# Kernel optimization log

Hardware: AMD Instinct MI355X
Metric: run time of the kernel (lower is better)

The kernel has to match this reference:

```python
import jax, jax.numpy as jnp
import numpy as np

IN_SHAPE, OUT_SHAPE = 512, 2048  # folding3 config from BSANet


def _sample_2d(m, n):
    # Faithful port of BSANet.sample_2D: 46x46 grid over [-0.3, 0.3]^2
    xs = np.linspace(-0.3, 0.3, 46)
    pts = np.stack(np.meshgrid(xs, xs))                    # [2, 46, 46]
    ix = np.round(np.linspace(0, 45, m)).astype(int)
    iy = np.round(np.linspace(0, 45, n)).astype(int)
    gx, gy = np.meshgrid(ix, iy)                           # each [n, m]
    return jnp.asarray(pts[:, gx.ravel(), gy.ravel()].T, jnp.float32)  # [m*n, 2]


def _lin(x, W, b):
    # MLP() in the source is Linear followed by ReLU for EVERY layer
    return jax.nn.relu(x @ W + b)


def setup_inputs() -> dict:
    key = jax.random.key(0)
    ks = jax.random.split(key, 20)
    def w(k, i, o):
        return jax.random.normal(k, (i, o), jnp.float32) / np.float32(np.sqrt(i))
    def bvec(k, o):
        return jax.random.normal(k, (o,), jnp.float32) * 0.01
    return {
        "p": jax.random.normal(ks[0], (32, IN_SHAPE, 128), jnp.float32),
        # SelfAttention MLPs (shared by both Up_module calls, as in the source)
        "Wh": w(ks[1], 256, 64),   "bh": bvec(ks[2], 64),
        "Wl": w(ks[3], 256, 64),   "bl": bvec(ks[4], 64),
        "Wg": w(ks[5], 256, 256),  "bg": bvec(ks[6], 256),
        "Wf": w(ks[7], 256, 128),  "bf": bvec(ks[8], 128),
        # M_up: MLP([130, 128])
        "Wup": w(ks[9], 130, 128), "bup": bvec(ks[10], 128),
        # M_down: MLP([512, 256, 128])
        "Wd1": w(ks[11], 512, 256), "bd1": bvec(ks[12], 256),
        "Wd2": w(ks[13], 256, 128), "bd2": bvec(ks[14], 128),
        "m": 64,
        "n": 32,
    }


def reference(p, Wh, bh, Wl, bl, Wg, bg, Wf, bf, Wup, bup, Wd1, bd1, Wd2, bd2, m, n):
    r = OUT_SHAPE // IN_SHAPE                              # 4
    pts = _sample_2d(m, n)                                 # [2048, 2]

    def up(q):                                             # q: [B, 512, 128]
        q = jnp.tile(q, (1, r, 1))                         # [B, 2048, 128] (torch repeat along dim 1)
        grid = jnp.broadcast_to(pts, (q.shape[0],) + pts.shape)
        q2d = _lin(jnp.concatenate([q, grid], -1), Wup, bup)   # [B, 2048, 128]
        qc = jnp.concatenate([q, q2d], -1)                 # [B, 2048, 256]
        h = _lin(qc, Wh, bh)                               # [B, 2048, 64]
        l = _lin(qc, Wl, bl)                               # [B, 2048, 64]
        g = _lin(qc, Wg, bg)                               # [B, 2048, 256]
        attn = jax.nn.softmax(jnp.einsum('bnd,bmd->bnm', l, h), axis=-1)  # [B, 2048, 2048]
        return _lin(qc + jnp.einsum('bnm,bmd->bnd', attn, g), Wf, bf)     # [B, 2048, 128]

    def down(q):                                           # q: [B, 2048, 128]
        q = q.reshape(q.shape[0], IN_SHAPE, r * q.shape[2])  # [B, 512, 512]
        return _lin(_lin(q, Wd1, bd1), Wd2, bd2)           # [B, 512, 128]

    p1 = up(p)
    p2 = up(p - down(p1))
    return p1 + p2
```

## Files before the change

### kernel.cpp

```cpp
#include <hip/hip_runtime.h>
#include <hip/hip_bf16.h>
#include <cmath>

#define NB   32
#define SOUT 2048
#define SIN  512
#define LOG2E 1.4426950408889634f

typedef __attribute__((ext_vector_type(8))) short bhalf8;
typedef __attribute__((ext_vector_type(4))) float f32x4;

__device__ inline ushort f2b(float x) {
  union { float f; unsigned u; } v; v.f = x;
  unsigned r = v.u + 0x7FFFu + ((v.u >> 16) & 1u);
  return (ushort)(r >> 16);
}
__device__ inline float b2f(ushort u) {
  union { unsigned u; float f; } v; v.u = ((unsigned)u) << 16;
  return v.f;
}
__device__ inline unsigned pkt(float lo, float hi) {
  union { float f; unsigned u; } a, b; a.f = lo; b.f = hi;
  return (a.u >> 16) | (b.u & 0xFFFF0000u);
}

__device__ inline void gload16(const void* g, void* l) {
  __builtin_amdgcn_global_load_lds(
      (const __attribute__((address_space(1))) void*)g,
      (__attribute__((address_space(3))) void*)l, 16, 0, 0);
}

__global__ void pts_kernel(const int* __restrict__ mArr, const int* __restrict__ nArr,
                           float* __restrict__ pts) {
  int k = blockIdx.x * blockDim.x + threadIdx.x;
  if (k >= SOUT) return;
  int m = mArr[0], n = nArr[0];
  int b = k % m, a = k / m;
  int ixb = (int)rint(45.0 * (double)b / (double)(m - 1));
  int iya = (int)rint(45.0 * (double)a / (double)(n - 1));
  const float step = 0.6f / 45.0f;
  pts[2 * k + 0] = -0.3f + step * (float)iya;
  pts[2 * k + 1] = -0.3f + step * (float)ixb;
}

__global__ __launch_bounds__(256) void wconv_kernel(
    const float* __restrict__ Wh, const float* __restrict__ Wl,
    const float* __restrict__ Wg, const float* __restrict__ Wf,
    const float* __restrict__ Wd1, const float* __restrict__ Wd2,
    const float* __restrict__ bh, const float* __restrict__ bl,
    const float* __restrict__ bg, const float* __restrict__ Wup,
    const float* __restrict__ bup, const float* __restrict__ pts,
    ushort* __restrict__ dst, float* __restrict__ fbias,
    float* __restrict__ gridterm) {
  const int which = blockIdx.y;
  int idx = blockIdx.x * 256 + threadIdx.x;
  if (which == 6) {
    if (idx < 384)
      fbias[idx] = idx < 64 ? bh[idx] : (idx < 128 ? bl[idx - 64] : bg[idx - 128]);
    return;
  }
  if (which == 7) {
    if (idx < 2048 * 128) {
      int i = idx >> 7, n = idx & 127;
      gridterm[idx] = bup[n] + pts[2 * i] * Wup[128 * 128 + n]
                             + pts[2 * i + 1] * Wup[129 * 128 + n];
    }
    return;
  }
  if (which == 8) {
    if (idx < 16384) {
      int n = idx >> 7, k = idx & 127;
      dst[294912 + n * 128 + k] = f2b(Wup[k * 128 + n]);
    }
    return;
  }
  const float* src; int K, N; long off;
  switch (which) {
    case 0: src = Wh;  K = 256; N = 64;  off = 0;      break;
    case 1: src = Wl;  K = 256; N = 64;  off = 16384;  break;
    case 2: src = Wg;  K = 256; N = 256; off = 32768;  break;
    case 3: src = Wf;  K = 256; N = 128; off = 98304;  break;
    case 4: src = Wd1; K = 512; N = 256; off = 131072; break;
    default:src = Wd2; K = 256; N = 128; off = 262144; break;
  }
  if (idx >= K * N) return;
  int n = idx / K, k = idx - n * K;
  dst[off + idx] = f2b(src[(long)k * N + n]);
}

__global__ __launch_bounds__(256) void pconv_kernel(
    const float* __restrict__ p, ushort* __restrict__ pb,
    ushort* __restrict__ qcb) {
  int idx = blockIdx.x * 256 + threadIdx.x;
  long base = (long)idx * 4;
  int b = (int)(base >> 16);
  int rem = (int)(base & 65535);
  int i = rem >> 7, n = rem & 127;
  float4 v = *(const float4*)(p + base);
  ushort4 u;
  u.x = f2b(v.x); u.y = f2b(v.y); u.z = f2b(v.z); u.w = f2b(v.w);
  *(ushort4*)(pb + base) = u;
#pragma unroll
  for (int j = 0; j < 4; ++j)
    *(ushort4*)(qcb + ((long)b * 2048 + i + 512 * j) * 256 + n) = u;
}

template <int MODE>
__global__ __launch_bounds__(256) void mgemm(
    const ushort* __restrict__ A, const ushort* __restrict__ Wt,
    const float* __restrict__ bias, void* __restrict__ outv,
    void* __restrict__ out2v, const float* __restrict__ aux,
    int M, int N, int K) {
  __shared__ alignas(16) ushort As[128 * 64];
  __shared__ alignas(16) ushort Bs[64 * 64];
  const int tid = threadIdx.x;
  const int w = tid >> 6, lane = tid & 63, g = lane >> 4, c = lane & 15;
  const int wm = w >> 1, wn = w & 1;
  const long row0 = (long)blockIdx.y * 128;
  const int col0 = blockIdx.x * 64;
  const long Astride = (long)K * 2;
  const char* Wb = (const char*)Wt;
  const long abase = (MODE == 6) ? ((row0 >> 11) * 512 + (row0 & 511)) : row0;
  const char* Ab = (const char*)A + abase * Astride;

  f32x4 acc[4][2];
#pragma unroll
  for (int i = 0; i < 4; ++i)
#pragma unroll
    for (int j = 0; j < 2; ++j) acc[i][j] = (f32x4){0.f, 0.f, 0.f, 0.f};

  for (int k0 = 0; k0 < K; k0 += 64) {
#pragma unroll
    for (int it = 0; it < 4; ++it) {
      int o = it * 4096 + w * 1024 + lane * 16;
      int row = o >> 7, cb = o & 127;
      gload16(Ab + (long)row * Astride + k0 * 2 + (cb ^ ((row & 7) << 4)),
              (char*)As + it * 4096 + w * 1024);
    }
#pragma unroll
    for (int it = 0; it < 2; ++it) {
      int o = it * 4096 + w * 1024 + lane * 16;
      int row = o >> 7, cb = o & 127;
      gload16(Wb + (long)(col0 + row) * Astride + k0 * 2 + (cb ^ ((row & 7) << 4)),
              (char*)Bs + it * 4096 + w * 1024);
    }
    __syncthreads();
#pragma unroll
    for (int koff = 0; koff < 2; ++koff) {
      bhalf8 a[4], bfr[2];
#pragma unroll
      for (int mi = 0; mi < 4; ++mi) {
        int row = 64 * wm + 16 * mi + c;
        a[mi] = *(const bhalf8*)((const char*)As + row * 128 +
                                 ((16 * g + 64 * koff) ^ ((row & 7) << 4)));
      }
#pragma unroll
      for (int ni = 0; ni < 2; ++ni) {
        int row = 32 * wn + 16 * ni + c;
        bfr[ni] = *(const bhalf8*)((const char*)Bs + row * 128 +
                                   ((16 * g + 64 * koff) ^ ((row & 7) << 4)));
      }
#pragma unroll
      for (int mi = 0; mi < 4; ++mi)
#pragma unroll
        for (int ni = 0; ni < 2; ++ni)
          acc[mi][ni] = __builtin_amdgcn_mfma_f32_16x16x32_bf16(a[mi], bfr[ni], acc[mi][ni], 0, 0, 0);
    }
    __syncthreads();
  }

#pragma unroll
  for (int ni = 0; ni < 2; ++ni) {
    int n = col0 + 32 * wn + 16 * ni + c;
    float bn = (MODE == 6) ? 0.f : bias[n];
#pragma unroll
    for (int mi = 0; mi < 4; ++mi) {
      long m0 = row0 + 64 * wm + 16 * mi + 4 * g;
      if (MODE == 6) {
        ushort* O = (ushort*)outv;
#pragma unroll
        for (int r = 0; r < 4; ++r) {
          int i2048 = (int)((m0 + r) & 2047);
          float val = fmaxf(acc[mi][ni][r] + aux[i2048 * 128 + n], 0.f);
          O[(m0 + r) * 256 + 128 + n] = f2b(val);
        }
        continue;
      }
      float v[4];
#pragma unroll
      for (int r = 0; r < 4; ++r) v[r] = fmaxf(acc[mi][ni][r] + bn, 0.f);
      if (MODE == 0) {
        ushort* O = (ushort*)outv;
#pragma unroll
        for (int r = 0; r < 4; ++r) O[(m0 + r) * N + n] = f2b(v[r]);
      } else if (MODE == 7) {
        if (n < 128) {
          ushort* O = (ushort*)outv;
          float sc = (n >= 64) ? LOG2E : 1.0f;
#pragma unroll
          for (int r = 0; r < 4; ++r) O[(m0 + r) * 128 + n] = f2b(v[r] * sc);
        } else {
          int bb = (int)(m0 >> 11);
          int ml = (int)(m0 & 2047);
          int d = n - 128;
          ushort4 u4;
          u4.x = f2b(v[0]); u4.y = f2b(v[1]); u4.z = f2b(v[2]); u4.w = f2b(v[3]);
          *(ushort4*)((ushort*)out2v + ((long)bb * 256 + d) * 2048 + ml) = u4;
        }
      } else if (MODE == 2) {
        ushort* O = (ushort*)outv;
        float* O2 = (float*)out2v;
#pragma unroll
        for (int r = 0; r < 4; ++r) {
          O2[(m0 + r) * N + n] = v[r];
          O[(m0 + r) * N + n] = f2b(v[r]);
        }
      } else if (MODE == 3) {
        ushort* Opmb = (ushort*)outv;
        ushort* Oqcb = (ushort*)out2v;
#pragma unroll
        for (int r = 0; r < 4; ++r) {
          float val = aux[(m0 + r) * N + n] - v[r];
          ushort uv = f2b(val);
          Opmb[(m0 + r) * 128 + n] = uv;
          long bb = (m0 + r) >> 9;
          int ii = (int)((m0 + r) & 511);
#pragma unroll
          for (int j = 0; j < 4; ++j)
            Oqcb[(bb * 2048 + ii + 512 * j) * 256 + n] = uv;
        }
      } else {
        float* O = (float*)outv;
#pragma unroll
        for (int r = 0; r < 4; ++r) O[(m0 + r) * N + n] = v[r] + aux[(m0 + r) * N + n];
      }
    }
  }
}

__global__ __launch_bounds__(256, 2) void attn_kernel(
    const ushort* __restrict__ hl, const ushort* __restrict__ gtm,
    ushort* __restrict__ qcb) {
  __shared__ alignas(16) ushort Ht[2][64 * 64];
  __shared__ alignas(16) ushort Gs[2][256 * 64];

  const int tid = threadIdx.x;
  const int w = tid >> 6, lane = tid & 63, g = lane >> 4, c = lane & 15;
  const int bid = blockIdx.x;
  const int wg = (bid & 7) * 64 + (bid >> 3);
  const int b = wg >> 4, nb = wg & 15;
  const float THR = 11.0f;

  bhalf8 la[2][2];
#pragma unroll
  for (int qg = 0; qg < 2; ++qg) {
    const ushort* lrow = hl + ((long)b * SOUT + nb * 128 + 32 * w + 16 * qg + c) * 128 + 64 + 8 * g;
    la[qg][0] = *(const bhalf8*)(lrow);
    la[qg][1] = *(const bhalf8*)(lrow + 32);
  }

  float mold[2] = {-INFINITY, -INFINITY}, srow[2] = {0.f, 0.f};
  f32x4 oacc[16][2];
#pragma unroll
  for (int t = 0; t < 16; ++t)
#pragma unroll
    for (int qg = 0; qg < 2; ++qg) oacc[t][qg] = (f32x4){0.f, 0.f, 0.f, 0.f};

  const char* hlbase = (const char*)(hl + (long)b * SOUT * 128);
  const char* gtb = (const char*)(gtm + (long)b * 256 * 2048);

  {
#pragma unroll
    for (int it = 0; it < 2; ++it) {
      int o = it * 4096 + tid * 16;
      int row = o >> 7, cb = o & 127;
      gload16(hlbase + row * 256 + (cb ^ ((row & 7) << 4)), (char*)Ht[0] + o);
    }
#pragma unroll
    for (int it = 0; it < 8; ++it) {
      int o = it * 4096 + tid * 16;
      int row = o >> 7, cb = o & 127;
      gload16(gtb + (long)row * 4096 + (cb ^ ((row & 7) << 4)), (char*)Gs[0] + o);
    }
  }
  __syncthreads();

  const int srcA = c + 32 * (g & 1);
  const int srcB = srcA + 16;
  const bool hi = (g >> 1) != 0;

  for (int mb = 0; mb < 32; ++mb) {
    const int buf = mb & 1;

    if (mb < 31) {
#pragma unroll
      for (int it = 0; it < 2; ++it) {
        int o = it * 4096 + tid * 16;
        int row = o >> 7, cb = o & 127;
        gload16(hlbase + ((long)(mb + 1) * 64 + row) * 256 + (cb ^ ((row & 7) << 4)),
                (char*)Ht[buf ^ 1] + o);
      }
#pragma unroll
      for (int it = 0; it < 8; ++it) {
        int o = it * 4096 + tid * 16;
        int row = o >> 7, cb = o & 127;
        gload16(gtb + (long)row * 4096 + (mb + 1) * 128 + (cb ^ ((row & 7) << 4)),
                (char*)Gs[buf ^ 1] + o);
      }
    }

    const char* hcur = (const char*)Ht[buf];
    f32x4 sacc[2][4];
#pragma unroll
    for (int qg = 0; qg < 2; ++qg)
#pragma unroll
      for (int j = 0; j < 4; ++j) sacc[qg][j] = (f32x4){0.f, 0.f, 0.f, 0.f};
#pragma unroll
    for (int j = 0; j < 4; ++j) {
      int row = 16 * j + c;
#pragma unroll
      for (int s = 0; s < 2; ++s) {
        bhalf8 hbf = *(const bhalf8*)(hcur + row * 128 +
                                      ((64 * s + 16 * g) ^ ((c & 7) << 4)));
        sacc[0][j] = __builtin_amdgcn_mfma_f32_16x16x32_bf16(hbf, la[0][s], sacc[0][j], 0, 0, 0);
        sacc[1][j] = __builtin_amdgcn_mfma_f32_16x16x32_bf16(hbf, la[1][s], sacc[1][j], 0, 0, 0);
      }
    }

    bhalf8 pb[2][2];
#pragma unroll
    for (int qg = 0; qg < 2; ++qg) {
      float mloc = sacc[qg][0][0];
#pragma unroll
      for (int j = 0; j < 4; ++j)
#pragma unroll
        for (int r = 0; r < 4; ++r) mloc = fmaxf(mloc, sacc[qg][j][r]);
      mloc = fmaxf(mloc, __shfl_xor(mloc, 16));
      mloc = fmaxf(mloc, __shfl_xor(mloc, 32));
      float mnew = fmaxf(mold[qg], mloc);
      bool keep = (mloc <= mold[qg] + THR);
      float scl = keep ? 1.0f : exp2f(mold[qg] - mnew);
      mold[qg] = keep ? mold[qg] : mnew;

      float psum = 0.f;
#pragma unroll
      for (int j = 0; j < 4; ++j)
#pragma unroll
        for (int r = 0; r < 4; ++r) {
          float e = exp2f(sacc[qg][j][r] - mold[qg]);
          sacc[qg][j][r] = e; psum += e;
        }
      psum += __shfl_xor(psum, 16);
      psum += __shfl_xor(psum, 32);
      srow[qg] = srow[qg] * scl + psum;
      if (!__all(keep)) {
#pragma unroll
        for (int t = 0; t < 16; ++t) {
          oacc[t][qg][0] *= scl; oacc[t][qg][1] *= scl;
          oacc[t][qg][2] *= scl; oacc[t][qg][3] *= scl;
        }
      }

#pragma unroll
      for (int s2 = 0; s2 < 2; ++s2) {
        int j2 = 2 * s2;
        unsigned wA0 = pkt(sacc[qg][j2][0], sacc[qg][j2][1]);
        unsigned wA1 = pkt(sacc[qg][j2][2], sacc[qg][j2][3]);
        unsigned wB0 = pkt(sacc[qg][j2 + 1][0], sacc[qg][j2 + 1][1]);
        unsigned wB1 = pkt(sacc[qg][j2 + 1][2], sacc[qg][j2 + 1][3]);
        unsigned a0A = (unsigned)__shfl((int)wA0, srcA);
        unsigned b0A = (unsigned)__shfl((int)wB0, srcA);
        unsigned a1A = (unsigned)__shfl((int)wA1, srcA);
        unsigned b1A = (unsigned)__shfl((int)wB1, srcA);
        unsigned a0B = (unsigned)__shfl((int)wA0, srcB);
        unsigned b0B = (unsigned)__shfl((int)wB0, srcB);
        unsigned a1B = (unsigned)__shfl((int)wA1, srcB);
        unsigned b1B = (unsigned)__shfl((int)wB1, srcB);
        union { unsigned u[4]; bhalf8 v; } pw;
        pw.u[0] = hi ? b0A : a0A;
        pw.u[1] = hi ? b1A : a1A;
        pw.u[2] = hi ? b0B : a0B;
        pw.u[3] = hi ? b1B : a1B;
        pb[qg][s2] = pw.v;
      }
    }

    const char* gcur = (const char*)Gs[buf];
#pragma unroll
    for (int s2 = 0; s2 < 2; ++s2) {
#pragma unroll
      for (int t = 0; t < 16; ++t) {
        int row = 16 * t + c;
        bhalf8 ga = *(const bhalf8*)(gcur + row * 128 +
                                     ((64 * s2 + 16 * g) ^ ((c & 7) << 4)));
        oacc[t][0] = __builtin_amdgcn_mfma_f32_16x16x32_bf16(ga, pb[0][s2], oacc[t][0], 0, 0, 0);
        oacc[t][1] = __builtin_amdgcn_mfma_f32_16x16x32_bf16(ga, pb[1][s2], oacc[t][1], 0, 0, 0);
      }
    }

    __syncthreads();
  }

#pragma unroll
  for (int qg = 0; qg < 2; ++qg) {
    float inv = 1.0f / srow[qg];
    long qrow = ((long)b * SOUT + nb * 128 + 32 * w + 16 * qg + c) * 256;
#pragma unroll
    for (int t = 0; t < 16; ++t) {
      long addr = qrow + 16 * t + 4 * g;
      ushort4 cur = *(const ushort4*)(qcb + addr);
      cur.x = f2b(b2f(cur.x) + oacc[t][qg][0] * inv);
      cur.y = f2b(b2f(cur.y) + oacc[t][qg][1] * inv);
      cur.z = f2b(b2f(cur.z) + oacc[t][qg][2] * inv);
      cur.w = f2b(b2f(cur.w) + oacc[t][qg][3] * inv);
      *(ushort4*)(qcb + addr) = cur;
    }
  }
}

extern "C" void kernel_launch(void* const* d_in, const int* in_sizes, int n_in,
                              void* d_out, int out_size, void* d_ws, size_t ws_size,
                              hipStream_t stream) {
  (void)in_sizes; (void)n_in; (void)out_size; (void)ws_size;
  const float* p   = (const float*)d_in[0];
  const float* Wh  = (const float*)d_in[1];
  const float* bh  = (const float*)d_in[2];
  const float* Wl  = (const float*)d_in[3];
  const float* bl  = (const float*)d_in[4];
  const float* Wg  = (const float*)d_in[5];
  const float* bg  = (const float*)d_in[6];
  const float* Wf  = (const float*)d_in[7];
  const float* bf  = (const float*)d_in[8];
  const float* Wup = (const float*)d_in[9];
  const float* bup = (const float*)d_in[10];
  const float* Wd1 = (const float*)d_in[11];
  const float* bd1 = (const float*)d_in[12];
  const float* Wd2 = (const float*)d_in[13];
  const float* bd2 = (const float*)d_in[14];
  const int* mArr  = (const int*)d_in[15];
  const int* nArr  = (const int*)d_in[16];
  float* out = (float*)d_out;

  float* ws       = (float*)d_ws;
  float* pts      = ws;
  float* p1       = ws + 4096;
  float* bhlg     = p1 + 8388608;
  float* gridterm = bhlg + 512;
  ushort* qcb  = (ushort*)(gridterm + 262144);
  ushort* hlb  = qcb + 16777216;
  ushort* gt   = hlb + 8388608;
  ushort* p1b  = gt + 16777216;
  ushort* d1b  = p1b + 8388608;
  ushort* pb   = d1b + 4194304;
  ushort* pmb  = pb + 2097152;
  ushort* wts  = pmb + 2097152;
  ushort* Wft  = wts + 98304;
  ushort* Wd1t = wts + 131072;
  ushort* Wd2t = wts + 262144;
  ushort* Wupt = wts + 294912;

  pts_kernel<<<8, 256, 0, stream>>>(mArr, nArr, pts);
  wconv_kernel<<<dim3(1024, 9), 256, 0, stream>>>(
      Wh, Wl, Wg, Wf, Wd1, Wd2, bh, bl, bg, Wup, bup, pts, wts, bhlg, gridterm);

  pconv_kernel<<<2048, 256, 0, stream>>>(p, pb, qcb);
  mgemm<6><<<dim3(2, 512), 256, 0, stream>>>(pb, Wupt, bhlg, qcb, nullptr, gridterm, 65536, 128, 128);
  mgemm<7><<<dim3(6, 512), 256, 0, stream>>>(qcb, wts, bhlg, hlb, gt, nullptr, 65536, 384, 256);
  attn_kernel<<<512, 256, 0, stream>>>(hlb, gt, qcb);
  mgemm<2><<<dim3(2, 512), 256, 0, stream>>>(qcb, Wft, bf, p1b, p1, nullptr, 65536, 128, 256);

  mgemm<0><<<dim3(4, 128), 256, 0, stream>>>(p1b, Wd1t, bd1, d1b, nullptr, nullptr, 16384, 256, 512);
  mgemm<3><<<dim3(2, 128), 256, 0, stream>>>(d1b, Wd2t, bd2, pmb, qcb, p, 16384, 128, 256);

  mgemm<6><<<dim3(2, 512), 256, 0, stream>>>(pmb, Wupt, bhlg, qcb, nullptr, gridterm, 65536, 128, 128);
  mgemm<7><<<dim3(6, 512), 256, 0, stream>>>(qcb, wts, bhlg, hlb, gt, nullptr, 65536, 384, 256);
  attn_kernel<<<512, 256, 0, stream>>>(hlb, gt, qcb);
  mgemm<4><<<dim3(2, 512), 256, 0, stream>>>(qcb, Wft, bf, out, p1, p1, 65536, 128, 256);
}
```

Baseline: 419.8 us.

## Single-buffer G tile in attention for higher occupancy; drop fp32 p1 copy

The attention kernel no longer double-buffers the 256x64 G tile in shared memory. It now loads G synchronously each iteration behind an extra barrier, which cuts LDS use and raises the launch-bounds occupancy target from 2 to 3 blocks per CU. The fp32 copy of p1 is also removed: the final GEMM adds the bf16 p1 instead, saving one fp32 write and read at some cost in precision. In exchange, the G load latency is no longer overlapped with the score computation and must be hidden by the extra occupancy.

```diff
diff --git a/kernel.cpp b/kernel.cpp
--- a/kernel.cpp
+++ b/kernel.cpp
@@ -207,14 +207,6 @@
           u4.x = f2b(v[0]); u4.y = f2b(v[1]); u4.z = f2b(v[2]); u4.w = f2b(v[3]);
           *(ushort4*)((ushort*)out2v + ((long)bb * 256 + d) * 2048 + ml) = u4;
         }
-      } else if (MODE == 2) {
-        ushort* O = (ushort*)outv;
-        float* O2 = (float*)out2v;
-#pragma unroll
-        for (int r = 0; r < 4; ++r) {
-          O2[(m0 + r) * N + n] = v[r];
-          O[(m0 + r) * N + n] = f2b(v[r]);
-        }
       } else if (MODE == 3) {
         ushort* Opmb = (ushort*)outv;
         ushort* Oqcb = (ushort*)out2v;
@@ -231,18 +223,20 @@
         }
       } else {
         float* O = (float*)outv;
-#pragma unroll
-        for (int r = 0; r < 4; ++r) O[(m0 + r) * N + n] = v[r] + aux[(m0 + r) * N + n];
-      }
-    }
-  }
-}
-
-__global__ __launch_bounds__(256, 2) void attn_kernel(
+        const ushort* auxb = (const ushort*)aux;
+#pragma unroll
+        for (int r = 0; r < 4; ++r)
+          O[(m0 + r) * N + n] = v[r] + b2f(auxb[(m0 + r) * N + n]);
+      }
+    }
+  }
+}
+
+__global__ __launch_bounds__(256, 3) void attn_kernel(
     const ushort* __restrict__ hl, const ushort* __restrict__ gtm,
     ushort* __restrict__ qcb) {
   __shared__ alignas(16) ushort Ht[2][64 * 64];
-  __shared__ alignas(16) ushort Gs[2][256 * 64];
+  __shared__ alignas(16) ushort Gs[256 * 64];
 
   const int tid = threadIdx.x;
   const int w = tid >> 6, lane = tid & 63, g = lane >> 4, c = lane & 15;
@@ -269,29 +263,28 @@
   const char* hlbase = (const char*)(hl + (long)b * SOUT * 128);
   const char* gtb = (const char*)(gtm + (long)b * 256 * 2048);
 
-  {
-#pragma unroll
-    for (int it = 0; it < 2; ++it) {
-      int o = it * 4096 + tid * 16;
-      int row = o >> 7, cb = o & 127;
-      gload16(hlbase + row * 256 + (cb ^ ((row & 7) << 4)), (char*)Ht[0] + o);
-    }
+#pragma unroll
+  for (int it = 0; it < 2; ++it) {
+    int o = it * 4096 + tid * 16;
+    int row = o >> 7, cb = o & 127;
+    gload16(hlbase + row * 256 + (cb ^ ((row & 7) << 4)), (char*)Ht[0] + o);
+  }
+  __syncthreads();
+
+  const int srcA = c + 32 * (g & 1);
+  const int srcB = srcA + 16;
+  const bool hi = (g >> 1) != 0;
+
+  for (int mb = 0; mb < 32; ++mb) {
+    const int buf = mb & 1;
+
 #pragma unroll
     for (int it = 0; it < 8; ++it) {
       int o = it * 4096 + tid * 16;
       int row = o >> 7, cb = o & 127;
-      gload16(gtb + (long)row * 4096 + (cb ^ ((row & 7) << 4)), (char*)Gs[0] + o);
-    }
-  }
-  __syncthreads();
-
-  const int srcA = c + 32 * (g & 1);
-  const int srcB = srcA + 16;
-  const bool hi = (g >> 1) != 0;
-
-  for (int mb = 0; mb < 32; ++mb) {
-    const int buf = mb & 1;
-
+      gload16(gtb + (long)row * 4096 + mb * 128 + (cb ^ ((row & 7) << 4)),
+              (char*)Gs + o);
+    }
     if (mb < 31) {
 #pragma unroll
       for (int it = 0; it < 2; ++it) {
@@ -299,13 +292,6 @@
         int row = o >> 7, cb = o & 127;
         gload16(hlbase + ((long)(mb + 1) * 64 + row) * 256 + (cb ^ ((row & 7) << 4)),
                 (char*)Ht[buf ^ 1] + o);
-      }
-#pragma unroll
-      for (int it = 0; it < 8; ++it) {
-        int o = it * 4096 + tid * 16;
-        int row = o >> 7, cb = o & 127;
-        gload16(gtb + (long)row * 4096 + (mb + 1) * 128 + (cb ^ ((row & 7) << 4)),
-                (char*)Gs[buf ^ 1] + o);
       }
     }
 
@@ -385,13 +371,14 @@
       }
     }
 
-    const char* gcur = (const char*)Gs[buf];
+    __syncthreads();
+
 #pragma unroll
     for (int s2 = 0; s2 < 2; ++s2) {
 #pragma unroll
       for (int t = 0; t < 16; ++t) {
         int row = 16 * t + c;
-        bhalf8 ga = *(const bhalf8*)(gcur + row * 128 +
+        bhalf8 ga = *(const bhalf8*)((const char*)Gs + row * 128 +
                                      ((64 * s2 + 16 * g) ^ ((c & 7) << 4)));
         oacc[t][0] = __builtin_amdgcn_mfma_f32_16x16x32_bf16(ga, pb[0][s2], oacc[t][0], 0, 0, 0);
         oacc[t][1] = __builtin_amdgcn_mfma_f32_16x16x32_bf16(ga, pb[1][s2], oacc[t][1], 0, 0, 0);
@@ -443,8 +430,7 @@
 
   float* ws       = (float*)d_ws;
   float* pts      = ws;
-  float* p1       = ws + 4096;
-  float* bhlg     = p1 + 8388608;
+  float* bhlg     = ws + 4096;
   float* gridterm = bhlg + 512;
   ushort* qcb  = (ushort*)(gridterm + 262144);
   ushort* hlb  = qcb + 16777216;
@@ -467,7 +453,7 @@
   mgemm<6><<<dim3(2, 512), 256, 0, stream>>>(pb, Wupt, bhlg, qcb, nullptr, gridterm, 65536, 128, 128);
   mgemm<7><<<dim3(6, 512), 256, 0, stream>>>(qcb, wts, bhlg, hlb, gt, nullptr, 65536, 384, 256);
   attn_kernel<<<512, 256, 0, stream>>>(hlb, gt, qcb);
-  mgemm<2><<<dim3(2, 512), 256, 0, stream>>>(qcb, Wft, bf, p1b, p1, nullptr, 65536, 128, 256);
+  mgemm<0><<<dim3(2, 512), 256, 0, stream>>>(qcb, Wft, bf, p1b, nullptr, nullptr, 65536, 128, 256);
 
   mgemm<0><<<dim3(4, 128), 256, 0, stream>>>(p1b, Wd1t, bd1, d1b, nullptr, nullptr, 16384, 256, 512);
   mgemm<3><<<dim3(2, 128), 256, 0, stream>>>(d1b, Wd2t, bd2, pmb, qcb, p, 16384, 128, 256);
@@ -475,5 +461,5 @@
   mgemm<6><<<dim3(2, 512), 256, 0, stream>>>(pmb, Wupt, bhlg, qcb, nullptr, gridterm, 65536, 128, 128);
   mgemm<7><<<dim3(6, 512), 256, 0, stream>>>(qcb, wts, bhlg, hlb, gt, nullptr, 65536, 384, 256);
   attn_kernel<<<512, 256, 0, stream>>>(hlb, gt, qcb);
-  mgemm<4><<<dim3(2, 512), 256, 0, stream>>>(qcb, Wft, bf, out, p1, p1, 65536, 128, 256);
-}
+  mgemm<8><<<dim3(2, 512), 256, 0, stream>>>(qcb, Wft, bf, out, nullptr, (const float*)p1b, 65536, 128, 256);
+}
```

After: 920.6 us. 2.19x slower.
